# Optimization experiments

Measured on AMD Instinct MI355X. Metric: run time of the kernel, lower is better.

## Reference

```python
import jax, jax.numpy as jnp
from jax import lax
import numpy as np

N, C_IN, C_OUT, H, W, D = 16, 32, 64, 128, 128, 5


def setup_inputs() -> dict:
    key = jax.random.key(0)
    k1, k2, k3, k4 = jax.random.split(key, 4)
    x = jax.random.normal(k1, (N, 1, C_IN, H, W), jnp.float32)
    d = jax.random.normal(k2, (N, C_OUT, C_IN, D, D), jnp.float32)
    y = jax.random.normal(k3, (N, C_OUT, 1, H, W), jnp.float32)
    alpha = jax.random.uniform(k4, (N, 1, 1, 1), jnp.float32)
    return {"x": x, "d": d, "y": y, "alpha": alpha, "reg": 1.0}


def _cross_corr(wts, img, pad):
    # out[i, j, u, v] = sum_{h,w} wts[i,h,w] * img[j, h+u-pad, w+v-pad]
    # (valid sums, zero padding). Implements the per-sample full-image conv3d
    # of the torch code (cross-correlation, no kernel flip).
    out = lax.conv_general_dilated(img[:, None], wts[:, None], (1, 1),
                                   [(pad, pad), (pad, pad)])
    return out.transpose(1, 0, 2, 3)  # (Ci_wts, Cj_img, 2*pad+1, 2*pad+1)


def reference(x, d, y, alpha, reg):
    n, _, c_in, h, w = x.shape
    c_out, ds = d.shape[1], d.shape[-1]
    K = c_in * ds * ds
    # Full autocorrelation R[n,c0,c1,a,b] = sum x[c0,h,w]*x[c1,h+a-(ds-1), w+b-(ds-1)]
    R = jax.vmap(lambda xn: _cross_corr(xn, xn, ds - 1))(x[:, 0])  # (n,C,C,2ds-1,2ds-1)
    # Toeplitz block assembly: Q[(c0,p,q),(c1,s,t)] = R[c0,c1, s-p+ds-1, t-q+ds-1]
    shift = jnp.arange(ds)[None, :] - jnp.arange(ds)[:, None] + (ds - 1)  # [p,s]
    Qa = R[:, :, :, shift, :]            # (n,c0,c1,p,s,2ds-1)
    Qb = Qa[..., shift]                  # (n,c0,c1,p,s,q,t)
    Q = Qb.transpose(0, 1, 3, 5, 2, 4, 6).reshape(n, K, K)
    # X^T y: S[n,o,c,u,v] = sum y[o,h,w]*x[c, h+u-p0, w+v-p0], p0=(ds-1)//2
    S = jax.vmap(lambda yn, xn: _cross_corr(yn, xn, (ds - 1) // 2))(y[:, :, 0], x[:, 0])
    P = S.transpose(0, 2, 3, 4, 1).reshape(n, K, c_out)
    # Tikhonov regularization around previous dictionary d
    a = alpha.reshape(n, 1) * (h * w * reg / (ds * ds * c_in))  # (n,1)
    Q = Q + a[:, :, None] * jnp.eye(K, dtype=Q.dtype)
    P = P + a[:, :, None] * d.reshape(n, c_out, K).transpose(0, 2, 1)
    # Batched Cholesky solve: D = Q^{-1} P
    L = jnp.linalg.cholesky(Q)
    z = lax.linalg.triangular_solve(L, P, left_side=True, lower=True)
    Dsol = lax.linalg.triangular_solve(L, z, left_side=True, lower=True, transpose_a=True)
    return Dsol.reshape(n, c_in, ds, ds, c_out).transpose(0, 4, 1, 2, 3)
```

## Files before the change

kernel.cpp:

```cpp
#include <hip/hip_runtime.h>

#define R_SZ    737280
#define Q_SZ    10240000
#define P_SZ    819200
#define LI_SZ   1024000
#define W_SZ    4608000

typedef unsigned short u16;
typedef __attribute__((ext_vector_type(8))) short bf16x8;
typedef __attribute__((ext_vector_type(4))) float f32x4;

#define MFMA16(a, b, c) __builtin_amdgcn_mfma_f32_16x16x32_bf16(a, b, c, 0, 0, 0)

__device__ __forceinline__ float alpha_scale(const float* alpha, const float* reg, int n) {
  return alpha[n] * (16384.0f * reg[0] / 800.0f);
}

__device__ __forceinline__ u16 f2bf(float f) {
  union { float f; unsigned u; } v; v.f = f;
  unsigned r = v.u + 0x7FFFu + ((v.u >> 16) & 1u);
  return (u16)(r >> 16);
}
__device__ __forceinline__ float bf2f(u16 h) {
  union { unsigned u; float f; } v; v.u = ((unsigned)h) << 16; return v.f;
}

__device__ __forceinline__ bf16x8 load8(const u16* p) {
  union { uint4 d; bf16x8 v; } u;
  u.d = *(const uint4*)p;
  return u.v;
}

__device__ __forceinline__ bf16x8 build_frag(const unsigned* w, int s) {
  union { unsigned u[4]; bf16x8 v; } f;
  int b = s >> 1;
  if (s & 1) {
    #pragma unroll
    for (int k = 0; k < 4; ++k) f.u[k] = (w[b + k] >> 16) | (w[b + k + 1] << 16);
  } else {
    #pragma unroll
    for (int k = 0; k < 4; ++k) f.u[k] = w[b + k];
  }
  return f.v;
}

__device__ __forceinline__ void stage_row(u16* slot, int partStride,
                                          const float* __restrict__ img,
                                          int C, int r, bool valid,
                                          int tid, int nthr) {
  for (int idx = tid; idx < C * 16; idx += nthr) {
    int c = idx >> 4, m = idx & 15;
    float v[8];
    if (valid) {
      const float* p = img + ((size_t)c * 128 + r) * 128 + m * 8;
      float4 a = *(const float4*)p;
      float4 b = *(const float4*)(p + 4);
      v[0]=a.x; v[1]=a.y; v[2]=a.z; v[3]=a.w; v[4]=b.x; v[5]=b.y; v[6]=b.z; v[7]=b.w;
    } else {
      #pragma unroll
      for (int k = 0; k < 8; ++k) v[k] = 0.0f;
    }
    union { u16 s[8]; uint2 d[2]; } hh, ll;
    #pragma unroll
    for (int k = 0; k < 8; ++k) {
      u16 h = f2bf(v[k]);
      hh.s[k] = h;
      ll.s[k] = f2bf(v[k] - bf2f(h));
    }
    u16* dh = slot + c * 136 + 4 + m * 8;
    *(uint2*)(dh)     = hh.d[0];
    *(uint2*)(dh + 4) = hh.d[1];
    u16* dl = dh + partStride;
    *(uint2*)(dl)     = ll.d[0];
    *(uint2*)(dl + 4) = ll.d[1];
  }
}

#define SLOT_US 8704
#define PSTR_32 4352
#define YPSTR   8704

__global__ __launch_bounds__(640) void k_corrR_mfma(const float* __restrict__ x,
                                                    float* __restrict__ Rpart) {
  __shared__ __align__(16) u16 lds[5 * SLOT_US];
  int n  = blockIdx.x >> 4;
  int r0 = (blockIdx.x & 15) << 3;
  int tid = threadIdx.x;
  const float* xn = x + (size_t)n * 32 * 128 * 128;

  if (tid < 320) {
    int s = tid / 64, p = (tid >> 5) & 1, c = tid & 31;
    u16* b = lds + s * SLOT_US + p * PSTR_32 + c * 136;
    uint2 z; z.x = 0; z.y = 0;
    *(uint2*)b = z;
    *(uint2*)(b + 132) = z;
  }
  for (int rr = 0; rr < 5; ++rr) {
    int r = r0 + rr;
    stage_row(lds + (r % 5) * SLOT_US, PSTR_32, xn, 32, r, r < 128, tid, 640);
  }

  int wave = tid >> 6, lane = tid & 63;
  int du = wave >> 1, nt = wave & 1;
  int lm = lane & 15, q = lane >> 4;

  f32x4 acc[9][2];
  #pragma unroll
  for (int dvi = 0; dvi < 9; ++dvi)
    #pragma unroll
    for (int mt = 0; mt < 2; ++mt) acc[dvi][mt] = (f32x4){0.f, 0.f, 0.f, 0.f};

  for (int i = r0; i < r0 + 8; ++i) {
    __syncthreads();
    const u16* A  = lds + (i % 5) * SLOT_US;
    const u16* Bp = lds + ((i + du) % 5) * SLOT_US;
    #pragma unroll
    for (int ks = 0; ks < 4; ++ks) {
      int kb = ks * 32 + q * 8;
      bf16x8 af[2][2];
      #pragma unroll
      for (int pa = 0; pa < 2; ++pa)
        #pragma unroll
        for (int mt = 0; mt < 2; ++mt)
          af[pa][mt] = load8(A + pa * PSTR_32 + (mt * 16 + lm) * 136 + 4 + kb);
      #pragma unroll
      for (int pb = 0; pb < 2; ++pb) {
        const u16* wp = Bp + pb * PSTR_32 + (nt * 16 + lm) * 136 + kb;
        uint4 w0 = *(const uint4*)wp;
        uint4 w1 = *(const uint4*)(wp + 8);
        unsigned w[8] = {w0.x, w0.y, w0.z, w0.w, w1.x, w1.y, w1.z, w1.w};
        #pragma unroll
        for (int dvi = 0; dvi < 9; ++dvi) {
          bf16x8 bf = build_frag(w, dvi);
          #pragma unroll
          for (int mt = 0; mt < 2; ++mt)
            #pragma unroll
            for (int pa = 0; pa < 2; ++pa) {
              if (pa == 1 && pb == 1) continue;
              acc[dvi][mt] = MFMA16(af[pa][mt], bf, acc[dvi][mt]);
            }
        }
      }
    }
    __syncthreads();
    if (i + 1 < r0 + 8) {
      int r = i + 5;
      stage_row(lds + (r % 5) * SLOT_US, PSTR_32, xn, 32, r, r < 128, tid, 640);
    }
  }

  float* Rp = Rpart + (size_t)blockIdx.x * 46080;
  #pragma unroll
  for (int dvi = 0; dvi < 9; ++dvi)
    #pragma unroll
    for (int mt = 0; mt < 2; ++mt) {
      float* dst = Rp + (du * 9 + dvi) * 1024 + (nt * 16 + lm) * 32 + mt * 16 + q * 4;
      *(f32x4*)dst = acc[dvi][mt];
    }
}

__global__ void k_reduceR(const float* __restrict__ part, float* __restrict__ R) {
  int idx = blockIdx.x * 256 + threadIdx.x;
  int n = idx / 46080, rem = idx % 46080;
  const float* p = part + (size_t)n * 16 * 46080 + rem;
  float s = 0.0f;
  #pragma unroll
  for (int c = 0; c < 16; ++c) s += p[(size_t)c * 46080];
  R[idx] = s;
}

__global__ __launch_bounds__(640) void k_corrP_mfma(const float* __restrict__ x,
                                                    const float* __restrict__ y,
                                                    float* __restrict__ Ppart) {
  __shared__ __align__(16) u16 xs[5 * SLOT_US];
  __shared__ __align__(16) u16 ys[2 * YPSTR];
  int n  = blockIdx.x >> 4;
  int r0 = (blockIdx.x & 15) << 3;
  int tid = threadIdx.x;
  const float* xn = x + (size_t)n * 32 * 128 * 128;
  const float* yn = y + (size_t)n * 64 * 128 * 128;

  if (tid < 320) {
    int s = tid / 64, p = (tid >> 5) & 1, c = tid & 31;
    u16* b = xs + s * SLOT_US + p * PSTR_32 + c * 136;
    uint2 z; z.x = 0; z.y = 0;
    *(uint2*)b = z;
    *(uint2*)(b + 132) = z;
  }
  for (int rr = -2; rr <= 2; ++rr) {
    int r = r0 + rr;
    stage_row(xs + ((r + 10) % 5) * SLOT_US, PSTR_32, xn, 32, r,
              (r >= 0 && r < 128), tid, 640);
  }
  stage_row(ys, YPSTR, yn, 64, r0, true, tid, 640);

  int wave = tid >> 6, lane = tid & 63;
  int du = (wave >> 1) - 2, mh = wave & 1;
  int lm = lane & 15, q = lane >> 4;

  f32x4 acc[5][2][2];
  #pragma unroll
  for (int dvi = 0; dvi < 5; ++dvi)
    #pragma unroll
    for (int mt = 0; mt < 2; ++mt)
      #pragma unroll
      for (int nt = 0; nt < 2; ++nt)
        acc[dvi][mt][nt] = (f32x4){0.f, 0.f, 0.f, 0.f};

  for (int i = r0; i < r0 + 8; ++i) {
    __syncthreads();
    const u16* Bp = xs + ((i + du + 10) % 5) * SLOT_US;
    #pragma unroll
    for (int ks = 0; ks < 4; ++ks) {
      int kb = ks * 32 + q * 8;
      bf16x8 af[2][2];
      #pragma unroll
      for (int pa = 0; pa < 2; ++pa)
        #pragma unroll
        for (int mt = 0; mt < 2; ++mt)
          af[pa][mt] = load8(ys + pa * YPSTR + (mh * 32 + mt * 16 + lm) * 136 + 4 + kb);
      #pragma unroll
      for (int nt = 0; nt < 2; ++nt)
        #pragma unroll
        for (int pb = 0; pb < 2; ++pb) {
          const u16* wp = Bp + pb * PSTR_32 + (nt * 16 + lm) * 136 + kb;
          uint4 w0 = *(const uint4*)wp;
          uint4 w1 = *(const uint4*)(wp + 8);
          unsigned w[8] = {w0.x, w0.y, w0.z, w0.w, w1.x, w1.y, w1.z, w1.w};
          #pragma unroll
          for (int dvi = 0; dvi < 5; ++dvi) {
            bf16x8 bf = build_frag(w, dvi + 2);
            #pragma unroll
            for (int mt = 0; mt < 2; ++mt)
              #pragma unroll
              for (int pa = 0; pa < 2; ++pa) {
                if (pa == 1 && pb == 1) continue;
                acc[dvi][mt][nt] = MFMA16(af[pa][mt], bf, acc[dvi][mt][nt]);
              }
          }
        }
    }
    __syncthreads();
    if (i + 1 < r0 + 8) {
      int r = i + 3;
      stage_row(xs + ((r + 10) % 5) * SLOT_US, PSTR_32, xn, 32, r,
                (r >= 0 && r < 128), tid, 640);
      stage_row(ys, YPSTR, yn, 64, i + 1, true, tid, 640);
    }
  }

  float* Pp = Ppart + (size_t)blockIdx.x * 51200;
  #pragma unroll
  for (int dvi = 0; dvi < 5; ++dvi)
    #pragma unroll
    for (int mt = 0; mt < 2; ++mt)
      #pragma unroll
      for (int nt = 0; nt < 2; ++nt) {
        float* dst = Pp + ((du + 2) * 5 + dvi) * 2048 + (nt * 16 + lm) * 64
                        + mh * 32 + mt * 16 + q * 4;
        *(f32x4*)dst = acc[dvi][mt][nt];
      }
}

__global__ void k_reduceP(const float* __restrict__ part, const float* __restrict__ d,
                          const float* __restrict__ alpha, const float* __restrict__ reg,
                          float* __restrict__ P) {
  int idx = blockIdx.x * 256 + threadIdx.x;
  int n = idx / 51200, rem = idx % 51200;
  int k = rem >> 6, co = rem & 63;
  int ci = k / 25, ae = k % 25;
  const float* p = part + (size_t)n * 16 * 51200 + (ae * 32 + ci) * 64 + co;
  float s = 0.0f;
  #pragma unroll
  for (int c = 0; c < 16; ++c) s += p[(size_t)c * 51200];
  float a = alpha_scale(alpha, reg, n);
  P[idx] = s + a * d[((size_t)n * 64 + co) * 800 + k];
}

__global__ void k_buildQ(const float* __restrict__ R, float* __restrict__ Q,
                         const float* __restrict__ alpha, const float* __restrict__ reg) {
  int bid = blockIdx.x;
  int n = bid / 800, k1 = bid % 800;
  int c1 = k1 / 25, r1 = k1 % 25, a = r1 / 5, e = r1 % 5;
  float av = alpha_scale(alpha, reg, n);
  const float* Rn = R + (size_t)n * 45 * 1024;
  float* Qrow = Q + ((size_t)n * 800 + k1) * 800;
  for (int k2 = threadIdx.x; k2 < 800; k2 += 256) {
    int c2 = k2 / 25, r2 = k2 % 25, b = r2 / 5, f = r2 % 5;
    int du = b - a, dv = f - e;
    float v = (du >= 0)
      ? Rn[(du * 9 + dv + 4) * 1024 + c2 * 32 + c1]
      : Rn[((-du) * 9 + 4 - dv) * 1024 + c1 * 32 + c2];
    if (k2 == k1) v += av;
    Qrow[k2] = v;
  }
}

#define DS 82

__device__ void diag_factor_invert2(float* As, float* Bs,
                                    float* __restrict__ Ln, float* __restrict__ LnT,
                                    int tid) {
  __shared__ float Dinv_s[16 * 25];
  for (int s = 0; s < 16; ++s) {
    int b = 5 * s;
    float a[5][5], dinv[5];
    #pragma unroll
    for (int ii = 0; ii < 5; ++ii)
      #pragma unroll
      for (int kk = 0; kk <= ii; ++kk) a[ii][kk] = As[(b+ii)*DS + b+kk];
    #pragma unroll
    for (int jj = 0; jj < 5; ++jj) {
      float dd = sqrtf(a[jj][jj]);
      a[jj][jj] = dd; dinv[jj] = 1.0f / dd;
      #pragma unroll
      for (int ii = jj+1; ii < 5; ++ii) a[ii][jj] *= dinv[jj];
      #pragma unroll
      for (int ii = jj+1; ii < 5; ++ii)
        #pragma unroll
        for (int kk = jj+1; kk <= ii; ++kk) a[ii][kk] -= a[ii][jj] * a[kk][jj];
    }
    if (tid < 25) {
      int ii = tid / 5, kk = tid % 5;
      if (kk <= ii) As[(b+ii)*DS + b+kk] = a[ii][kk];
    }
    int m = 75 - b;
    for (int r = tid; r < m; r += 256) {
      int row = b + 5 + r;
      float w[5];
      #pragma unroll
      for (int c = 0; c < 5; ++c) {
        float av2 = As[row*DS + b + c];
        #pragma unroll
        for (int kk = 0; kk < c; ++kk) av2 -= w[kk] * a[c][kk];
        w[c] = av2 * dinv[c];
      }
      #pragma unroll
      for (int c = 0; c < 5; ++c) As[row*DS + b + c] = w[c];
    }
    __syncthreads();
    for (int idx = tid; idx < m*m; idx += 256) {
      int ii = idx / m, kk = idx % m;
      if (kk <= ii) {
        int ri = b+5+ii, rk = b+5+kk;
        float acc2 = As[ri*DS + rk];
        #pragma unroll
        for (int c = 0; c < 5; ++c) acc2 -= As[ri*DS + b+c] * As[rk*DS + b+c];
        As[ri*DS + rk] = acc2;
      }
    }
    __syncthreads();
  }

  if (tid < 16) {
    int i = tid;
    const float* Ab = As + (5*i)*DS + 5*i;
    float L5[5][5], Di[5][5];
    #pragma unroll
    for (int r = 0; r < 5; ++r)
      #pragma unroll
      for (int c = 0; c <= r; ++c) L5[r][c] = Ab[r*DS + c];
    #pragma unroll
    for (int c = 0; c < 5; ++c) {
      #pragma unroll
      for (int r = 0; r < c; ++r) Di[r][c] = 0.0f;
      Di[c][c] = 1.0f / L5[c][c];
      #pragma unroll
      for (int r = c+1; r < 5; ++r) {
        float sacc = 0.0f;
        #pragma unroll
        for (int k = c; k < r; ++k) sacc += L5[r][k] * Di[k][c];
        Di[r][c] = -sacc * (1.0f / L5[r][r]);
      }
    }
    #pragma unroll
    for (int r = 0; r < 5; ++r)
      #pragma unroll
      for (int c = 0; c < 5; ++c) Dinv_s[i*25 + r*5 + c] = Di[r][c];
  }
  __syncthreads();

  if (tid < 80) {
    int j = tid;
    for (int i = 0; i < 16; ++i) {
      float bv[5];
      #pragma unroll
      for (int r = 0; r < 5; ++r) bv[r] = (5*i + r == j) ? 1.0f : 0.0f;
      const float* Arow = As + (5*i)*DS;
      #pragma unroll 5
      for (int k = 0; k < 5*i; ++k) {
        float xc = Bs[k*DS + j];
        #pragma unroll
        for (int r = 0; r < 5; ++r) bv[r] -= Arow[r*DS + k] * xc;
      }
      #pragma unroll
      for (int r = 0; r < 5; ++r) {
        float v = 0.0f;
        #pragma unroll
        for (int c = 0; c <= r; ++c) v += Dinv_s[i*25 + r*5 + c] * bv[c];
        Bs[(5*i + r)*DS + j] = v;
      }
    }
  }
  __syncthreads();
  for (int idx = tid; idx < 6400; idx += 256) {
    int r = idx / 80, c = idx % 80;
    float v = (r >= c) ? Bs[r*DS + c] : 0.0f;
    Ln[idx] = v;
    LnT[c*80 + r] = v;
  }
}

__global__ __launch_bounds__(256) void k_diag0(const float* __restrict__ Q,
                                               float* __restrict__ Linv,
                                               float* __restrict__ LinvT) {
  __shared__ float As[80*DS];
  __shared__ float Bs[80*DS];
  int n = blockIdx.x, tid = threadIdx.x;
  const float* Qn = Q + (size_t)n * 640000;
  for (int idx = tid; idx < 6400; idx += 256) {
    int r = idx / 80, c = idx % 80;
    As[r*DS + c] = Qn[r*800 + c];
  }
  __syncthreads();
  diag_factor_invert2(As, Bs, Linv + (size_t)n*10*6400, LinvT + (size_t)n*10*6400, tid);
}

__global__ __launch_bounds__(256) void k_panel(const float* __restrict__ Q,
                                               const float* __restrict__ Linv,
                                               float* __restrict__ Wrm,
                                               float* __restrict__ Wcm,
                                               int t) {
  int nt = 9 - t;
  int n = blockIdx.x / nt;
  int s = blockIdx.x % nt;
  int bu = t + 1 + s;

  __shared__ float Ls[80*DS];
  __shared__ float Aa[80*DS];
  int tid = threadIdx.x, tc = tid & 15, tr = tid >> 4;
  const float* Qn = Q + (size_t)n * 640000;
  const float* Ln = Linv + ((size_t)n*10 + t) * 6400;

  for (int idx = tid; idx < 6400; idx += 256) {
    int r = idx / 80, c = idx % 80;
    Ls[r*DS + c] = Ln[idx];
    Aa[r*DS + c] = Qn[(size_t)(80*bu + r)*800 + 80*t + c];
  }
  __syncthreads();

  float acc[5][5];
  #pragma unroll
  for (int a = 0; a < 5; ++a)
    #pragma unroll
    for (int b = 0; b < 5; ++b) acc[a][b] = 0.0f;
  for (int k = 0; k < 80; ++k) {
    float av[5], bv[5];
    #pragma unroll
    for (int dd = 0; dd < 5; ++dd) { av[dd] = Aa[(5*tr+dd)*DS + k]; bv[dd] = Ls[(5*tc+dd)*DS + k]; }
    #pragma unroll
    for (int a = 0; a < 5; ++a)
      #pragma unroll
      for (int b = 0; b < 5; ++b) acc[a][b] += av[a] * bv[b];
  }

  int p = t*9 - t*(t-1)/2 + s;
  size_t base = ((size_t)n*45 + p) * 6400;
  #pragma unroll
  for (int a = 0; a < 5; ++a)
    #pragma unroll
    for (int b = 0; b < 5; ++b) {
      Wrm[base + (5*tr+a)*80 + 5*tc+b] = acc[a][b];
      Wcm[base + (5*tc+b)*80 + 5*tr+a] = acc[a][b];
    }
}

__global__ __launch_bounds__(256) void k_trail(float* __restrict__ Q,
                                               float* __restrict__ Linv,
                                               float* __restrict__ LinvT,
                                               const float* __restrict__ Wrm,
                                               int t) {
  int nt = 9 - t;
  int T = nt * (nt + 1) / 2;
  int n = blockIdx.x / T;
  int rr = blockIdx.x % T;
  int i = 0;
  while (rr >= i + 1) { rr -= i + 1; ++i; }
  int j = rr;
  int bi = t + 1 + i, bj = t + 1 + j;

  __shared__ float Wi[80*DS];
  __shared__ float Wj[80*DS];
  __shared__ float As[80*DS];
  int tid = threadIdx.x, tc = tid & 15, tr = tid >> 4;
  float* Qn = Q + (size_t)n * 640000;
  int pb = t*9 - t*(t-1)/2;
  const float* Wri = Wrm + ((size_t)n*45 + pb + i) * 6400;
  const float* Wrj = Wrm + ((size_t)n*45 + pb + j) * 6400;

  for (int idx = tid; idx < 6400; idx += 256) {
    int r = idx / 80, c = idx % 80;
    Wi[r*DS + c] = Wri[idx];
    As[r*DS + c] = Qn[(size_t)(80*bi + r)*800 + 80*bj + c];
  }
  if (i != j) {
    for (int idx = tid; idx < 6400; idx += 256) {
      int r = idx / 80, c = idx % 80;
      Wj[r*DS + c] = Wrj[idx];
    }
  }
  __syncthreads();

  const float* Wjb = (i != j) ? Wj : Wi;
  float acc[5][5];
  #pragma unroll
  for (int a = 0; a < 5; ++a)
    #pragma unroll
    for (int b = 0; b < 5; ++b) acc[a][b] = 0.0f;
  for (int k = 0; k < 80; ++k) {
    float av[5], bv[5];
    #pragma unroll
    for (int dd = 0; dd < 5; ++dd) { av[dd] = Wi[(5*tr+dd)*DS + k]; bv[dd] = Wjb[(5*tc+dd)*DS + k]; }
    #pragma unroll
    for (int a = 0; a < 5; ++a)
      #pragma unroll
      for (int b = 0; b < 5; ++b) acc[a][b] += av[a] * bv[b];
  }

  bool special = (i == 0 && j == 0);
  if (!special) {
    #pragma unroll
    for (int a = 0; a < 5; ++a)
      #pragma unroll
      for (int b = 0; b < 5; ++b)
        Qn[(size_t)(80*bi + 5*tr+a)*800 + 80*bj + 5*tc+b] =
          As[(5*tr+a)*DS + 5*tc+b] - acc[a][b];
  } else {
    #pragma unroll
    for (int a = 0; a < 5; ++a)
      #pragma unroll
      for (int b = 0; b < 5; ++b)
        As[(5*tr+a)*DS + 5*tc+b] -= acc[a][b];
    __syncthreads();
    diag_factor_invert2(As, Wj,
                        Linv  + ((size_t)n*10 + t + 1) * 6400,
                        LinvT + ((size_t)n*10 + t + 1) * 6400, tid);
  }
}

#define ZS 20

__device__ __forceinline__ void seg80p(const float* __restrict__ Mcur, int i,
                                       const float* __restrict__ Mnext,
                                       float4 (&A)[8],
                                       const float2 (&zc)[80],
                                       float& a0, float& a1) {
  const float* Ci = Mcur + i * 80;
  const float* Ni = Mnext + i * 80;
  #pragma unroll
  for (int h = 0; h < 20; ++h) {
    float4 v = A[h & 7];
    if (h < 12)      A[h & 7]  = *(const float4*)(Ci + 4 * (h + 8));
    else if (h < 16) A[h - 8]  = *(const float4*)(Ni + 4 * (h - 8));
    else             A[h - 16] = *(const float4*)(Ni + 4 * (h - 16));
    a0 += v.x * zc[4*h].x;     a1 += v.x * zc[4*h].y;
    a0 += v.y * zc[4*h + 1].x; a1 += v.y * zc[4*h + 1].y;
    a0 += v.z * zc[4*h + 2].x; a1 += v.z * zc[4*h + 2].y;
    a0 += v.w * zc[4*h + 3].x; a1 += v.w * zc[4*h + 3].y;
  }
}

__global__ __launch_bounds__(160, 1) void k_solve(const float* __restrict__ Linv,
                                                  const float* __restrict__ LinvT,
                                                  const float* __restrict__ Wrm,
                                                  const float* __restrict__ Wcm,
                                                  const float* __restrict__ P,
                                                  float* __restrict__ out) {
  __shared__ __align__(16) float z2[2 * 800 * 2];
  int bid = blockIdx.x;
  int sub = bid >> 3;
  int n   = (bid & 7) * 2 + (sub >> 4);
  int qg4 = (sub & 15) << 2;
  int tid = threadIdx.x;
  int i   = tid % 80;
  int cp  = tid / 80;
  const float* Lb  = Linv  + (size_t)n * 10 * 6400;
  const float* LTb = LinvT + (size_t)n * 10 * 6400;
  const float* Wr  = Wrm + (size_t)n * 45 * 6400;
  const float* Wc  = Wcm + (size_t)n * 45 * 6400;

  for (int idx = tid; idx < 3200; idx += 160) {
    int k = idx >> 2, cc = idx & 3;
    z2[((cc >> 1) * 800 + k) * 2 + (cc & 1)] =
        P[((size_t)n * 800 + k) * 64 + qg4 + cc];
  }

  float2 zc[80];
  float4 A[8];
  {
    const float* Mi = Lb + i * 80;
    #pragma unroll
    for (int q = 0; q < 8; ++q) A[q] = *(const float4*)(Mi + 4 * q);
  }

  for (int t = 0; t < 10; ++t) {
    __syncthreads();
    int zb = (cp * 800 + 80 * t) * 2;
    #pragma unroll
    for (int m = 0; m < 40; ++m) {
      float4 v = *(const float4*)&z2[zb + 4 * m];
      zc[2*m]     = make_float2(v.x, v.y);
      zc[2*m + 1] = make_float2(v.z, v.w);
    }
    int nseg = 9 - t;
    const float* Mc = Wr + (size_t)(t * 9 - t * (t - 1) / 2) * 6400;
    const float* nxt = (nseg > 0) ? Mc
                      : (t < 9 ? Lb + (t + 1) * 6400 : LTb + 9 * 6400);
    float a0 = 0.f, a1 = 0.f;
    seg80p(Lb + t * 6400, i, nxt, A, zc, a0, a1);
    __syncthreads();
    *(float2*)&z2[(cp * 800 + 80 * t + i) * 2] = make_float2(a0, a1);
    __syncthreads();
    #pragma unroll
    for (int m = 0; m < 40; ++m) {
      float4 v = *(const float4*)&z2[zb + 4 * m];
      zc[2*m]     = make_float2(v.x, v.y);
      zc[2*m + 1] = make_float2(v.z, v.w);
    }
    for (int s = 0; s < nseg; ++s) {
      const float* nx2 = (s + 1 < nseg) ? Mc + (size_t)(s + 1) * 6400
                                        : Lb + (t + 1) * 6400;
      float b0 = 0.f, b1 = 0.f;
      seg80p(Mc + (size_t)s * 6400, i, nx2, A, zc, b0, b1);
      float2* zp = (float2*)&z2[(cp * 800 + 80 * (t + 1 + s) + i) * 2];
      float2 v = *zp; v.x -= b0; v.y -= b1; *zp = v;
    }
  }

  for (int t = 9; t >= 0; --t) {
    __syncthreads();
    int zb = (cp * 800 + 80 * t) * 2;
    #pragma unroll
    for (int m = 0; m < 40; ++m) {
      float4 v = *(const float4*)&z2[zb + 4 * m];
      zc[2*m]     = make_float2(v.x, v.y);
      zc[2*m + 1] = make_float2(v.z, v.w);
    }
    const float* nxt;
    if (t > 0) {
      int p0 = (t - 1) * 9 - (t - 1) * (t - 2) / 2;
      nxt = Wc + (size_t)p0 * 6400;
    } else nxt = Lb;
    float a0 = 0.f, a1 = 0.f;
    seg80p(LTb + t * 6400, i, nxt, A, zc, a0, a1);
    __syncthreads();
    *(float2*)&z2[(cp * 800 + 80 * t + i) * 2] = make_float2(a0, a1);
    __syncthreads();
    #pragma unroll
    for (int m = 0; m < 40; ++m) {
      float4 v = *(const float4*)&z2[zb + 4 * m];
      zc[2*m]     = make_float2(v.x, v.y);
      zc[2*m + 1] = make_float2(v.z, v.w);
    }
    for (int u = t - 1; u >= 0; --u) {
      int p = u * 9 - u * (u - 1) / 2 + (t - u - 1);
      const float* nx2;
      if (u > 0) {
        int pn = (u - 1) * 9 - (u - 1) * (u - 2) / 2 + (t - u);
        nx2 = Wc + (size_t)pn * 6400;
      } else nx2 = (t > 0) ? LTb + (t - 1) * 6400 : Lb;
      float b0 = 0.f, b1 = 0.f;
      seg80p(Wc + (size_t)p * 6400, i, nx2, A, zc, b0, b1);
      float2* zp = (float2*)&z2[(cp * 800 + 80 * u + i) * 2];
      float2 v = *zp; v.x -= b0; v.y -= b1; *zp = v;
    }
  }

  __syncthreads();
  for (int idx = tid; idx < 3200; idx += 160) {
    int c = idx / 800, k = idx % 800;
    out[((size_t)n * 64 + qg4 + c) * 800 + k] =
        z2[((c >> 1) * 800 + k) * 2 + (c & 1)];
  }
}

extern "C" void kernel_launch(void* const* d_in, const int* in_sizes, int n_in,
                              void* d_out, int out_size, void* d_ws, size_t ws_size,
                              hipStream_t stream) {
  const float* x     = (const float*)d_in[0];
  const float* d     = (const float*)d_in[1];
  const float* y     = (const float*)d_in[2];
  const float* alpha = (const float*)d_in[3];
  const float* reg   = (const float*)d_in[4];
  float* out = (float*)d_out;
  float* ws  = (float*)d_ws;

  float* R    = ws;
  float* Q    = R + R_SZ;
  float* P    = Q + Q_SZ;
  float* Li   = P + P_SZ;
  float* part = Li + LI_SZ;
  float* LiT  = part;
  float* Wrm  = part + LI_SZ;
  float* Wcm  = Wrm + W_SZ;

  k_corrR_mfma<<<256, 640, 0, stream>>>(x, part);
  k_reduceR<<<R_SZ / 256, 256, 0, stream>>>(part, R);
  k_corrP_mfma<<<256, 640, 0, stream>>>(x, y, part);
  k_reduceP<<<P_SZ / 256, 256, 0, stream>>>(part, d, alpha, reg, P);
  k_buildQ<<<16 * 800, 256, 0, stream>>>(R, Q, alpha, reg);

  k_diag0<<<16, 256, 0, stream>>>(Q, Li, LiT);
  for (int t = 0; t < 9; ++t) {
    int nt = 9 - t;
    k_panel<<<16 * nt, 256, 0, stream>>>(Q, Li, Wrm, Wcm, t);
    k_trail<<<16 * nt * (nt + 1) / 2, 256, 0, stream>>>(Q, Li, LiT, Wrm, t);
  }

  k_solve<<<16 * 16, 160, 0, stream>>>(Li, LiT, Wrm, Wcm, P, out);
}
```

Measured before the change: 1.334 ms.

## Restructure block solve to chunk z and issue all segment loads together

The solve kernel used a software-pipelined seg80p helper that prefetched the next 80x80 block row through a rotating register buffer, processing off-diagonal segments one at a time. Now each off-diagonal update loops over four 20-wide chunks of z and issues loads for all remaining segments (up to 9) within each chunk, keeping nine accumulator pairs in registers. The aim is more independent memory loads in flight per thread instead of a serial prefetch chain, and fewer live zc registers (20 instead of 80). The cost is more accumulator registers and the loss of cross-block prefetch at the diagonal step.

Measured after the change: 1.526 ms. 14.3% more time.

```diff
diff --git a/kernel.cpp b/kernel.cpp
--- a/kernel.cpp
+++ b/kernel.cpp
@@ -545,28 +545,6 @@
     diag_factor_invert2(As, Wj,
                         Linv  + ((size_t)n*10 + t + 1) * 6400,
                         LinvT + ((size_t)n*10 + t + 1) * 6400, tid);
-  }
-}
-
-#define ZS 20
-
-__device__ __forceinline__ void seg80p(const float* __restrict__ Mcur, int i,
-                                       const float* __restrict__ Mnext,
-                                       float4 (&A)[8],
-                                       const float2 (&zc)[80],
-                                       float& a0, float& a1) {
-  const float* Ci = Mcur + i * 80;
-  const float* Ni = Mnext + i * 80;
-  #pragma unroll
-  for (int h = 0; h < 20; ++h) {
-    float4 v = A[h & 7];
-    if (h < 12)      A[h & 7]  = *(const float4*)(Ci + 4 * (h + 8));
-    else if (h < 16) A[h - 8]  = *(const float4*)(Ni + 4 * (h - 8));
-    else             A[h - 16] = *(const float4*)(Ni + 4 * (h - 16));
-    a0 += v.x * zc[4*h].x;     a1 += v.x * zc[4*h].y;
-    a0 += v.y * zc[4*h + 1].x; a1 += v.y * zc[4*h + 1].y;
-    a0 += v.z * zc[4*h + 2].x; a1 += v.z * zc[4*h + 2].y;
-    a0 += v.w * zc[4*h + 3].x; a1 += v.w * zc[4*h + 3].y;
   }
 }
 
@@ -595,84 +573,149 @@
         P[((size_t)n * 800 + k) * 64 + qg4 + cc];
   }
 
-  float2 zc[80];
-  float4 A[8];
-  {
-    const float* Mi = Lb + i * 80;
-    #pragma unroll
-    for (int q = 0; q < 8; ++q) A[q] = *(const float4*)(Mi + 4 * q);
-  }
-
   for (int t = 0; t < 10; ++t) {
     __syncthreads();
     int zb = (cp * 800 + 80 * t) * 2;
-    #pragma unroll
-    for (int m = 0; m < 40; ++m) {
-      float4 v = *(const float4*)&z2[zb + 4 * m];
-      zc[2*m]     = make_float2(v.x, v.y);
-      zc[2*m + 1] = make_float2(v.z, v.w);
-    }
+    float a0 = 0.f, a1 = 0.f;
+    {
+      const float* Mi = Lb + t * 6400 + i * 80;
+      #pragma unroll
+      for (int c = 0; c < 4; ++c) {
+        float2 zc[20];
+        #pragma unroll
+        for (int m = 0; m < 10; ++m) {
+          float4 v = *(const float4*)&z2[zb + c * 40 + 4 * m];
+          zc[2*m]     = make_float2(v.x, v.y);
+          zc[2*m + 1] = make_float2(v.z, v.w);
+        }
+        float4 mv[5];
+        #pragma unroll
+        for (int q = 0; q < 5; ++q) mv[q] = *(const float4*)(Mi + c * 20 + 4 * q);
+        #pragma unroll
+        for (int q = 0; q < 5; ++q) {
+          a0 += mv[q].x * zc[4*q].x;     a1 += mv[q].x * zc[4*q].y;
+          a0 += mv[q].y * zc[4*q + 1].x; a1 += mv[q].y * zc[4*q + 1].y;
+          a0 += mv[q].z * zc[4*q + 2].x; a1 += mv[q].z * zc[4*q + 2].y;
+          a0 += mv[q].w * zc[4*q + 3].x; a1 += mv[q].w * zc[4*q + 3].y;
+        }
+      }
+    }
+    __syncthreads();
+    *(float2*)&z2[(cp * 800 + 80 * t + i) * 2] = make_float2(a0, a1);
+    __syncthreads();
     int nseg = 9 - t;
-    const float* Mc = Wr + (size_t)(t * 9 - t * (t - 1) / 2) * 6400;
-    const float* nxt = (nseg > 0) ? Mc
-                      : (t < 9 ? Lb + (t + 1) * 6400 : LTb + 9 * 6400);
+    if (nseg > 0) {
+      const float* Mc = Wr + (size_t)(t * 9 - t * (t - 1) / 2) * 6400 + i * 80;
+      float acc[9][2];
+      #pragma unroll
+      for (int s = 0; s < 9; ++s) { acc[s][0] = 0.f; acc[s][1] = 0.f; }
+      #pragma unroll
+      for (int c = 0; c < 4; ++c) {
+        float2 zc[20];
+        #pragma unroll
+        for (int m = 0; m < 10; ++m) {
+          float4 v = *(const float4*)&z2[zb + c * 40 + 4 * m];
+          zc[2*m]     = make_float2(v.x, v.y);
+          zc[2*m + 1] = make_float2(v.z, v.w);
+        }
+        #pragma unroll
+        for (int s = 0; s < 9; ++s) {
+          if (s < nseg) {
+            const float* Ms = Mc + (size_t)s * 6400 + c * 20;
+            float4 mv[5];
+            #pragma unroll
+            for (int q = 0; q < 5; ++q) mv[q] = *(const float4*)(Ms + 4 * q);
+            #pragma unroll
+            for (int q = 0; q < 5; ++q) {
+              acc[s][0] += mv[q].x * zc[4*q].x;     acc[s][1] += mv[q].x * zc[4*q].y;
+              acc[s][0] += mv[q].y * zc[4*q + 1].x; acc[s][1] += mv[q].y * zc[4*q + 1].y;
+              acc[s][0] += mv[q].z * zc[4*q + 2].x; acc[s][1] += mv[q].z * zc[4*q + 2].y;
+              acc[s][0] += mv[q].w * zc[4*q + 3].x; acc[s][1] += mv[q].w * zc[4*q + 3].y;
+            }
+          }
+        }
+      }
+      #pragma unroll
+      for (int s = 0; s < 9; ++s) {
+        if (s < nseg) {
+          float2* zp = (float2*)&z2[(cp * 800 + 80 * (t + 1 + s) + i) * 2];
+          float2 v = *zp; v.x -= acc[s][0]; v.y -= acc[s][1]; *zp = v;
+        }
+      }
+    }
+  }
+
+  for (int t = 9; t >= 0; --t) {
+    __syncthreads();
+    int zb = (cp * 800 + 80 * t) * 2;
     float a0 = 0.f, a1 = 0.f;
-    seg80p(Lb + t * 6400, i, nxt, A, zc, a0, a1);
+    {
+      const float* Mi = LTb + t * 6400 + i * 80;
+      #pragma unroll
+      for (int c = 0; c < 4; ++c) {
+        float2 zc[20];
+        #pragma unroll
+        for (int m = 0; m < 10; ++m) {
+          float4 v = *(const float4*)&z2[zb + c * 40 + 4 * m];
+          zc[2*m]     = make_float2(v.x, v.y);
+          zc[2*m + 1] = make_float2(v.z, v.w);
+        }
+        float4 mv[5];
+        #pragma unroll
+        for (int q = 0; q < 5; ++q) mv[q] = *(const float4*)(Mi + c * 20 + 4 * q);
+        #pragma unroll
+        for (int q = 0; q < 5; ++q) {
+          a0 += mv[q].x * zc[4*q].x;     a1 += mv[q].x * zc[4*q].y;
+          a0 += mv[q].y * zc[4*q + 1].x; a1 += mv[q].y * zc[4*q + 1].y;
+          a0 += mv[q].z * zc[4*q + 2].x; a1 += mv[q].z * zc[4*q + 2].y;
+          a0 += mv[q].w * zc[4*q + 3].x; a1 += mv[q].w * zc[4*q + 3].y;
+        }
+      }
+    }
     __syncthreads();
     *(float2*)&z2[(cp * 800 + 80 * t + i) * 2] = make_float2(a0, a1);
     __syncthreads();
-    #pragma unroll
-    for (int m = 0; m < 40; ++m) {
-      float4 v = *(const float4*)&z2[zb + 4 * m];
-      zc[2*m]     = make_float2(v.x, v.y);
-      zc[2*m + 1] = make_float2(v.z, v.w);
-    }
-    for (int s = 0; s < nseg; ++s) {
-      const float* nx2 = (s + 1 < nseg) ? Mc + (size_t)(s + 1) * 6400
-                                        : Lb + (t + 1) * 6400;
-      float b0 = 0.f, b1 = 0.f;
-      seg80p(Mc + (size_t)s * 6400, i, nx2, A, zc, b0, b1);
-      float2* zp = (float2*)&z2[(cp * 800 + 80 * (t + 1 + s) + i) * 2];
-      float2 v = *zp; v.x -= b0; v.y -= b1; *zp = v;
-    }
-  }
-
-  for (int t = 9; t >= 0; --t) {
-    __syncthreads();
-    int zb = (cp * 800 + 80 * t) * 2;
-    #pragma unroll
-    for (int m = 0; m < 40; ++m) {
-      float4 v = *(const float4*)&z2[zb + 4 * m];
-      zc[2*m]     = make_float2(v.x, v.y);
-      zc[2*m + 1] = make_float2(v.z, v.w);
-    }
-    const float* nxt;
-    if (t > 0) {
-      int p0 = (t - 1) * 9 - (t - 1) * (t - 2) / 2;
-      nxt = Wc + (size_t)p0 * 6400;
-    } else nxt = Lb;
-    float a0 = 0.f, a1 = 0.f;
-    seg80p(LTb + t * 6400, i, nxt, A, zc, a0, a1);
-    __syncthreads();
-    *(float2*)&z2[(cp * 800 + 80 * t + i) * 2] = make_float2(a0, a1);
-    __syncthreads();
-    #pragma unroll
-    for (int m = 0; m < 40; ++m) {
-      float4 v = *(const float4*)&z2[zb + 4 * m];
-      zc[2*m]     = make_float2(v.x, v.y);
-      zc[2*m + 1] = make_float2(v.z, v.w);
-    }
-    for (int u = t - 1; u >= 0; --u) {
-      int p = u * 9 - u * (u - 1) / 2 + (t - u - 1);
-      const float* nx2;
-      if (u > 0) {
-        int pn = (u - 1) * 9 - (u - 1) * (u - 2) / 2 + (t - u);
-        nx2 = Wc + (size_t)pn * 6400;
-      } else nx2 = (t > 0) ? LTb + (t - 1) * 6400 : Lb;
-      float b0 = 0.f, b1 = 0.f;
-      seg80p(Wc + (size_t)p * 6400, i, nx2, A, zc, b0, b1);
-      float2* zp = (float2*)&z2[(cp * 800 + 80 * u + i) * 2];
-      float2 v = *zp; v.x -= b0; v.y -= b1; *zp = v;
+    int nseg = t;
+    if (nseg > 0) {
+      float acc[9][2];
+      #pragma unroll
+      for (int s = 0; s < 9; ++s) { acc[s][0] = 0.f; acc[s][1] = 0.f; }
+      #pragma unroll
+      for (int c = 0; c < 4; ++c) {
+        float2 zc[20];
+        #pragma unroll
+        for (int m = 0; m < 10; ++m) {
+          float4 v = *(const float4*)&z2[zb + c * 40 + 4 * m];
+          zc[2*m]     = make_float2(v.x, v.y);
+          zc[2*m + 1] = make_float2(v.z, v.w);
+        }
+        #pragma unroll
+        for (int s = 0; s < 9; ++s) {
+          if (s < nseg) {
+            int u = t - 1 - s;
+            int p = u * 9 - u * (u - 1) / 2 + (t - u - 1);
+            const float* Ms = Wc + (size_t)p * 6400 + i * 80 + c * 20;
+            float4 mv[5];
+            #pragma unroll
+            for (int q = 0; q < 5; ++q) mv[q] = *(const float4*)(Ms + 4 * q);
+            #pragma unroll
+            for (int q = 0; q < 5; ++q) {
+              acc[s][0] += mv[q].x * zc[4*q].x;     acc[s][1] += mv[q].x * zc[4*q].y;
+              acc[s][0] += mv[q].y * zc[4*q + 1].x; acc[s][1] += mv[q].y * zc[4*q + 1].y;
+              acc[s][0] += mv[q].z * zc[4*q + 2].x; acc[s][1] += mv[q].z * zc[4*q + 2].y;
+              acc[s][0] += mv[q].w * zc[4*q + 3].x; acc[s][1] += mv[q].w * zc[4*q + 3].y;
+            }
+          }
+        }
+      }
+      #pragma unroll
+      for (int s = 0; s < 9; ++s) {
+        if (s < nseg) {
+          int u = t - 1 - s;
+          float2* zp = (float2*)&z2[(cp * 800 + 80 * u + i) * 2];
+          float2 v = *zp; v.x -= acc[s][0]; v.y -= acc[s][1]; *zp = v;
+        }
+      }
     }
   }
 
```
